# Kernel tuning notes

Measured on AMD Instinct MI355X. Metric: run time of the kernel, lower is better.

The kernel has to match this reference:

```python
import jax, jax.numpy as jnp
import numpy as np

TOPK = 13
ALPHA = 1.0
BETA = 6.0
NUM_CLASSES = 80
EPS = 1e-9


def _make_boxes(key, shape, max_half):
    # shape = (..., 4): build valid x1y1x2y2 boxes inside a 640x640 image
    kc, ks = jax.random.split(key)
    centers = jax.random.uniform(kc, shape[:-1] + (2,), minval=30.0, maxval=610.0)
    halves = jax.random.uniform(ks, shape[:-1] + (2,), minval=2.0, maxval=max_half)
    return jnp.concatenate([centers - halves, centers + halves], axis=-1)


def setup_inputs() -> dict:
    key = jax.random.key(0)
    k1, k2, k3, k4, k5 = jax.random.split(key, 5)
    B, L, C, n = 16, 8400, NUM_CLASSES, 128
    pred_scores = jax.random.uniform(k1, (B, L, C), dtype=jnp.float32)
    pred_bboxes = _make_boxes(k2, (B, L, 4), 60.0)
    anchor_points = jax.random.uniform(k3, (L, 2), minval=0.0, maxval=640.0)
    gt_labels = jax.random.randint(k4, (B, n), 0, C, dtype=jnp.int32)
    gt_bboxes = _make_boxes(k5, (B, n, 4), 120.0)
    pad_gt_mask = jnp.ones((B, n, 1), dtype=jnp.float32)
    return {"pred_scores": pred_scores, "pred_bboxes": pred_bboxes,
            "anchor_points": anchor_points, "gt_labels": gt_labels,
            "gt_bboxes": gt_bboxes, "pad_gt_mask": pad_gt_mask}


def _batch_iou(box1, box2, eps=1e-9):
    # box1: [B, n, 4], box2: [B, L, 4] -> iou [B, n, L]
    b1 = box1[:, :, None]  # [B,n,1,4]
    b2 = box2[:, None]     # [B,1,L,4]
    x1y1 = jnp.maximum(b1[..., 0:2], b2[..., 0:2])
    x2y2 = jnp.minimum(b1[..., 2:4], b2[..., 2:4])
    overlap = jnp.prod(jnp.clip(x2y2 - x1y1, 0.0), axis=-1)
    area1 = jnp.prod(jnp.clip(b1[..., 2:4] - b1[..., 0:2], 0.0), axis=-1)
    area2 = jnp.prod(jnp.clip(b2[..., 2:4] - b2[..., 0:2], 0.0), axis=-1)
    return overlap / (area1 + area2 - overlap + eps)


def _points_in_bboxes(points, bboxes, eps=EPS):
    # points: [L,2], bboxes: [B,n,4] -> [B,n,L] float
    x = points[None, None, :, 0]
    y = points[None, None, :, 1]
    xmin = bboxes[..., 0:1]; ymin = bboxes[..., 1:2]
    xmax = bboxes[..., 2:3]; ymax = bboxes[..., 3:4]
    l = x - xmin; t = y - ymin; r = xmax - x; b = ymax - y
    d = jnp.minimum(jnp.minimum(l, t), jnp.minimum(r, b))
    return (d > eps).astype(bboxes.dtype)


def _gather_topk(metrics, topk, topk_mask):
    # metrics: [B,n,L] -> one-hot membership of per-gt topk anchors [B,n,L]
    L = metrics.shape[-1]
    _, topk_idxs = jax.lax.top_k(metrics, topk)          # [B,n,topk]
    is_in_topk = jax.nn.one_hot(topk_idxs, L, dtype=metrics.dtype).sum(-2)
    return is_in_topk * topk_mask


def reference(pred_scores, pred_bboxes, anchor_points, gt_labels, gt_bboxes, pad_gt_mask):
    B, n, _ = gt_bboxes.shape
    L = pred_bboxes.shape[1]
    # pairwise IoU between gts and predicted boxes: [B,n,L]
    ious = _batch_iou(gt_bboxes, pred_bboxes)
    # per-gt class scores gathered from pred_scores: [B,n,L]
    scores_cl = jnp.transpose(pred_scores, (0, 2, 1))                 # [B,C,L]
    bbox_cls_scores = jnp.take_along_axis(scores_cl, gt_labels[:, :, None].astype(jnp.int32), axis=1)
    # task-aligned metric
    alignment = (bbox_cls_scores ** ALPHA) * (ious ** BETA)
    is_in_gts = _points_in_bboxes(anchor_points, gt_bboxes)           # [B,n,L]
    is_in_topk = _gather_topk(alignment * is_in_gts, TOPK, pad_gt_mask)
    mask_positive = is_in_topk * is_in_gts * pad_gt_mask              # [B,n,L]
    # resolve anchors assigned to multiple gts: keep max-IoU gt
    mask_pos_sum = mask_positive.sum(-2)                              # [B,L]
    is_max_iou = jnp.transpose(jax.nn.one_hot(jnp.argmax(ious, axis=-2), n, dtype=ious.dtype), (0, 2, 1))
    mask_positive = jnp.where((mask_pos_sum[:, None, :] > 1), is_max_iou, mask_positive)
    mask_pos_sum = mask_positive.sum(-2)
    # assignment
    assigned_gt_index = jnp.argmax(mask_positive, axis=-2)            # [B,L]
    flat_idx = assigned_gt_index + jnp.arange(B, dtype=assigned_gt_index.dtype)[:, None] * n
    assigned_labels = jnp.reshape(gt_labels, (-1,))[flat_idx]
    assigned_labels = jnp.where(mask_pos_sum > 0, assigned_labels, NUM_CLASSES)
    assigned_bboxes = jnp.reshape(gt_bboxes, (-1, 4))[flat_idx]       # [B,L,4]
    assigned_scores = jax.nn.one_hot(assigned_labels, NUM_CLASSES + 1, dtype=pred_scores.dtype)[..., :NUM_CLASSES]
    # rescale scores by normalized alignment metric
    align_m = alignment * mask_positive
    max_metric = align_m.max(-1, keepdims=True)                       # [B,n,1]
    max_iou = (ious * mask_positive).max(-1, keepdims=True)           # [B,n,1]
    align_m = (align_m / (max_metric + EPS)) * max_iou
    assigned_scores = assigned_scores * align_m.max(-2)[..., None]    # [B,L,C]
    return assigned_labels, assigned_bboxes, assigned_scores
```

## Files before the change

kernel.cpp:

```cpp
#include <hip/hip_runtime.h>
#include <stdint.h>

#define BB   16
#define NGT  128
#define LL   8400
#define CC   80
#define KTOP 13
#define CAP  1024
#define FEPS 1e-9f

typedef float vfloat4 __attribute__((ext_vector_type(4)));

__device__ __forceinline__ float iou_f(float4 g, float4 p) {
    float ix0 = fmaxf(g.x, p.x);
    float iy0 = fmaxf(g.y, p.y);
    float ix1 = fminf(g.z, p.z);
    float iy1 = fminf(g.w, p.w);
    float ow = fmaxf(ix1 - ix0, 0.0f);
    float oh = fmaxf(iy1 - iy0, 0.0f);
    float ov = ow * oh;
    float a1 = fmaxf(g.z - g.x, 0.0f) * fmaxf(g.w - g.y, 0.0f);
    float a2 = fmaxf(p.z - p.x, 0.0f) * fmaxf(p.w - p.y, 0.0f);
    return ov / (a1 + a2 - ov + FEPS);
}

#define SORT2(a,b) { unsigned long long _t=(a), _u=(b); (a)=(_u>_t)?_u:_t; (b)=(_u>_t)?_t:_u; }
#define INSERT13(key) do { unsigned long long _k=(key); if (_k > k12) { k12=_k; \
    SORT2(k11,k12) SORT2(k10,k11) SORT2(k9,k10) SORT2(k8,k9) SORT2(k7,k8) \
    SORT2(k6,k7)  SORT2(k5,k6)  SORT2(k4,k5) SORT2(k3,k4) SORT2(k2,k3) \
    SORT2(k1,k2)  SORT2(k0,k1) } } while(0)
#define POP13() { k0=k1;k1=k2;k2=k3;k3=k4;k4=k5;k5=k6;k6=k7;k7=k8;k8=k9;k9=k10;k10=k11;k11=k12;k12=0ull; }

__global__ __launch_bounds__(256) void cand_kernel(
    const float*  __restrict__ pred_scores,
    const float4* __restrict__ pred_bboxes,
    const float2* __restrict__ anchors,
    const int*    __restrict__ gt_labels,
    const float4* __restrict__ gt_bboxes,
    unsigned long long* __restrict__ records,
    int* __restrict__ cand_cnt)
{
    int b  = blockIdx.y;
    int zi = blockIdx.z;
    int j  = blockIdx.x * 256 + threadIdx.x;

    __shared__ float4 gbox[8];
    __shared__ int    glab[8];
    if (threadIdx.x < 8) {
        gbox[threadIdx.x] = gt_bboxes[b * NGT + zi * 8 + threadIdx.x];
        glab[threadIdx.x] = gt_labels[b * NGT + zi * 8 + threadIdx.x];
    }
    __syncthreads();
    if (j >= LL) return;

    float2 ap = anchors[j];
    float4 p  = pred_bboxes[(size_t)b * LL + j];
    const float* srow = pred_scores + ((size_t)b * LL + j) * CC;

    unsigned mask = 0;
#pragma unroll
    for (int u = 0; u < 8; ++u) {
        float4 gg = gbox[u];
        float d  = fminf(fminf(ap.x - gg.x, ap.y - gg.y),
                         fminf(gg.z - ap.x, gg.w - ap.y));
        float io = iou_f(gg, p);
        mask |= ((d > FEPS) && (io > 0.0f)) ? (1u << u) : 0u;
    }

    while (mask) {
        int u = __ffs(mask) - 1;
        mask &= mask - 1;
        float4 gg = gbox[u];
        float io  = iou_f(gg, p);
        float s   = srow[glab[u]];
        float i2  = io * io;
        float met = s * (i2 * i2 * i2);
        if (met > 0.0f) {
            int rrow = b * NGT + zi * 8 + u;
            int slot = atomicAdd(cand_cnt + rrow, 1);
            if (slot < CAP)
                records[(size_t)rrow * CAP + slot] =
                    ((unsigned long long)__float_as_uint(met) << 32)
                    | (unsigned)(~(unsigned)j);
        }
    }
}

__global__ __launch_bounds__(64) void select_kernel(
    const float*  __restrict__ pred_scores,
    const float4* __restrict__ pred_bboxes,
    const float2* __restrict__ anchors,
    const int*    __restrict__ gt_labels,
    const float4* __restrict__ gt_bboxes,
    const unsigned long long* __restrict__ records,
    const int* __restrict__ cand_cnt,
    int force_fallback,
    int* __restrict__ claim_count,
    int* __restrict__ claimant)
{
    int lane = threadIdx.x;
    int row  = blockIdx.x;
    int b    = row >> 7;
    int i_gt = row & (NGT - 1);

    float4 g = gt_bboxes[row];
    unsigned long long k0=0,k1=0,k2=0,k3=0,k4=0,k5=0,k6=0,k7=0,k8=0,k9=0,k10=0,k11=0,k12=0;

    int cnt = cand_cnt[row];
    if (force_fallback || cnt > CAP) {
        int label = gt_labels[row];
        const float*  sc = pred_scores + (size_t)b * LL * CC + label;
        const float4* pb = pred_bboxes + (size_t)b * LL;
        for (int j = lane; j < LL; j += 64) {
            float2 ap = anchors[j];
            float d = fminf(fminf(ap.x - g.x, ap.y - g.y),
                            fminf(g.z - ap.x, g.w - ap.y));
            if (d > FEPS) {
                float4 p = pb[j];
                float iou = iou_f(g, p);
                if (iou > 0.0f) {
                    float s  = sc[(size_t)j * CC];
                    float i2 = iou * iou;
                    float met = s * (i2 * i2 * i2);
                    if (met > 0.0f)
                        INSERT13(((unsigned long long)__float_as_uint(met) << 32)
                                 | (unsigned)(~(unsigned)j));
                }
            }
        }
    } else {
        const unsigned long long* rr = records + (size_t)row * CAP;
        for (int t = lane; t < cnt; t += 64)
            INSERT13(rr[t]);
    }

    unsigned long long winner = 0ull;
    for (int r = 0; r < KTOP; ++r) {
        unsigned long long head = k0;
        unsigned long long m = head;
#pragma unroll
        for (int off = 1; off < 64; off <<= 1) {
            unsigned long long o = __shfl_xor(m, off, 64);
            if (o > m) m = o;
        }
        if (head == m && m != 0ull) {
            POP13();
        }
        if (lane == r) winner = m;
    }

    int jwv = -1;
    if (lane < KTOP && winner != 0ull)
        jwv = (int)(~(unsigned)(winner & 0xFFFFFFFFull));

    bool marked = false;
    for (int r = 0; r < KTOP; ++r) {
        int jv = __shfl(jwv, r, 64);
        if (jv == lane) marked = true;
    }
    unsigned long long nonpos = ~__ballot(marked);
    int P = __popcll(__ballot(jwv >= 0));

    int base = b * LL;
    if (jwv >= 0) {
        atomicAdd(claim_count + base + jwv, 1);
        atomicMax(claimant + base + jwv, i_gt);
    }
    if (lane >= P && lane < KTOP) {
        unsigned long long mask = nonpos;
        for (int t = 0; t < lane - P; ++t) mask &= mask - 1ull;
        int jf = __ffsll(mask) - 1;
        float2 ap = anchors[jf];
        float d = fminf(fminf(ap.x - g.x, ap.y - g.y),
                        fminf(g.z - ap.x, g.w - ap.y));
        if (d > FEPS) {
            atomicAdd(claim_count + base + jf, 1);
            atomicMax(claimant + base + jf, i_gt);
        }
    }
}

__global__ __launch_bounds__(256) void resolve_kernel(
    const float*  __restrict__ pred_scores,
    const float4* __restrict__ pred_bboxes,
    const int*    __restrict__ gt_labels,
    const float4* __restrict__ gt_bboxes,
    const int*    __restrict__ claim_count,
    const int*    __restrict__ claimant,
    int*      __restrict__ assigned_gt,
    float*    __restrict__ align_anchor,
    unsigned* __restrict__ max_metric,
    unsigned* __restrict__ max_iou,
    float*    __restrict__ out_labels,
    float4*   __restrict__ out_bboxes)
{
    int b = blockIdx.y;
    int j = blockIdx.x * 256 + threadIdx.x;

    __shared__ float4 gbox[NGT];
    __shared__ int    glab[NGT];
    if (threadIdx.x < NGT) {
        gbox[threadIdx.x] = gt_bboxes[b * NGT + threadIdx.x];
        glab[threadIdx.x] = gt_labels[b * NGT + threadIdx.x];
    }
    __syncthreads();
    if (j >= LL) return;

    int idx = b * LL + j;
    int cnt = claim_count[idx];
    int g = -1;
    float4 p = pred_bboxes[(size_t)b * LL + j];

    if (cnt == 1) {
        g = claimant[idx];
    } else if (cnt > 1) {
        float best = -1.0f;
        int   bi   = 0;
        for (int i = 0; i < NGT; ++i) {
            float iou = iou_f(gbox[i], p);
            if (iou > best) { best = iou; bi = i; }
        }
        g = bi;
    }
    assigned_gt[idx] = g;

    int label; float4 bb;
    if (g >= 0) {
        float iou = iou_f(gbox[g], p);
        float s   = pred_scores[((size_t)b * LL + j) * CC + glab[g]];
        float i2  = iou * iou;
        float al  = s * (i2 * i2 * i2);
        align_anchor[idx] = al;
        atomicMax(max_metric + b * NGT + g, __float_as_uint(al));
        atomicMax(max_iou    + b * NGT + g, __float_as_uint(iou));
        label = glab[g];
        bb    = gbox[g];
    } else {
        label = CC;
        bb    = gbox[0];
    }
    out_labels[idx] = (float)label;
    out_bboxes[idx] = bb;
}

__global__ __launch_bounds__(256) void score_kernel(
    const int*    __restrict__ gt_labels,
    const int*    __restrict__ assigned_gt,
    const float*  __restrict__ align_anchor,
    const unsigned* __restrict__ max_metric,
    const unsigned* __restrict__ max_iou,
    float*  __restrict__ out_scores)
{
    __shared__ int   s_lab[64];
    __shared__ float s_f[64];

    if (threadIdx.x < 64) {
        int t = blockIdx.x * 64 + threadIdx.x;
        int b = t / LL;
        int g = assigned_gt[t];
        int label = CC;
        float f = 0.0f;
        if (g >= 0) {
            label = gt_labels[b * NGT + g];
            float mm = __uint_as_float(max_metric[b * NGT + g]);
            float mi = __uint_as_float(max_iou[b * NGT + g]);
            f = align_anchor[t] / (mm + FEPS) * mi;
        }
        s_lab[threadIdx.x] = label;
        s_f[threadIdx.x]   = f;
    }
    __syncthreads();

    vfloat4* outs = (vfloat4*)(out_scores + (size_t)blockIdx.x * 64 * CC);
#pragma unroll
    for (int k = 0; k < 5; ++k) {
        int i = k * 256 + threadIdx.x;
        int anchor = i / (CC / 4);
        int c4     = i % (CC / 4);
        int lab    = s_lab[anchor];
        vfloat4 v = {0.f, 0.f, 0.f, 0.f};
        int rel = lab - c4 * 4;
        if (rel >= 0 && rel < 4) v[rel] = s_f[anchor];
        __builtin_nontemporal_store(v, outs + i);
    }
}

extern "C" void kernel_launch(void* const* d_in, const int* in_sizes, int n_in,
                              void* d_out, int out_size, void* d_ws, size_t ws_size,
                              hipStream_t stream)
{
    const float*  pred_scores = (const float*)d_in[0];
    const float4* pred_bboxes = (const float4*)d_in[1];
    const float2* anchors     = (const float2*)d_in[2];
    const int*    gt_labels   = (const int*)d_in[3];
    const float4* gt_bboxes   = (const float4*)d_in[4];

    char* w = (char*)d_ws;
    int*      claim_count  = (int*)(w);
    int*      claimant     = (int*)(w + 537600);
    unsigned* max_metric   = (unsigned*)(w + 1075200);
    unsigned* max_iou      = (unsigned*)(w + 1083392);
    int*      cand_cnt     = (int*)(w + 1091584);
    int*      assigned_gt  = (int*)(w + 1099776);
    float*    align_anchor = (float*)(w + 1637376);
    unsigned long long* records = (unsigned long long*)(w + 2174976);

    const size_t WS_NEEDED = 2174976ull + (size_t)BB * NGT * CAP * 8ull;
    int force_fallback = (ws_size < WS_NEEDED) ? 1 : 0;

    float*  out        = (float*)d_out;
    float*  out_labels = out;
    float4* out_bboxes = (float4*)(out + (size_t)BB * LL);
    float*  out_scores = out + (size_t)BB * LL * 5;

    (void)hipMemsetAsync(w, 0, 1099776, stream);

    if (!force_fallback) {
        dim3 gridG((LL + 255) / 256, BB, 16);
        cand_kernel<<<gridG, 256, 0, stream>>>(
            pred_scores, pred_bboxes, anchors, gt_labels, gt_bboxes,
            records, cand_cnt);
    }

    select_kernel<<<BB * NGT, 64, 0, stream>>>(
        pred_scores, pred_bboxes, anchors, gt_labels, gt_bboxes,
        records, cand_cnt, force_fallback, claim_count, claimant);

    dim3 gridC((LL + 255) / 256, BB);
    resolve_kernel<<<gridC, 256, 0, stream>>>(
        pred_scores, pred_bboxes, gt_labels, gt_bboxes,
        claim_count, claimant, assigned_gt, align_anchor, max_metric, max_iou,
        out_labels, out_bboxes);

    score_kernel<<<(BB * LL) / 64, 256, 0, stream>>>(
        gt_labels, assigned_gt, align_anchor, max_metric, max_iou, out_scores);
}
```

Baseline: 92.33 us.

## Remap candidate kernel to one thread per anchor-GT pair; use plain score stores

The candidate kernel's thread mapping changes from one thread per anchor looping over 8 GTs in shared memory to one thread per (anchor, GT) pair across all 128 GTs. The shared-memory staging and barrier go away, and the serial per-anchor loop is spread across lanes, at the cost of redundant anchor and pred_box loads and divergent branches inside each wavefront. Score output also switches from nontemporal stores to ordinary vector stores, which changes how the large output write interacts with the cache.

```diff
diff --git a/kernel.cpp b/kernel.cpp
--- a/kernel.cpp
+++ b/kernel.cpp
@@ -40,48 +40,31 @@
     unsigned long long* __restrict__ records,
     int* __restrict__ cand_cnt)
 {
-    int b  = blockIdx.y;
-    int zi = blockIdx.z;
-    int j  = blockIdx.x * 256 + threadIdx.x;
-
-    __shared__ float4 gbox[8];
-    __shared__ int    glab[8];
-    if (threadIdx.x < 8) {
-        gbox[threadIdx.x] = gt_bboxes[b * NGT + zi * 8 + threadIdx.x];
-        glab[threadIdx.x] = gt_labels[b * NGT + zi * 8 + threadIdx.x];
-    }
-    __syncthreads();
-    if (j >= LL) return;
-
-    float2 ap = anchors[j];
-    float4 p  = pred_bboxes[(size_t)b * LL + j];
-    const float* srow = pred_scores + ((size_t)b * LL + j) * CC;
-
-    unsigned mask = 0;
-#pragma unroll
-    for (int u = 0; u < 8; ++u) {
-        float4 gg = gbox[u];
-        float d  = fminf(fminf(ap.x - gg.x, ap.y - gg.y),
-                         fminf(gg.z - ap.x, gg.w - ap.y));
-        float io = iou_f(gg, p);
-        mask |= ((d > FEPS) && (io > 0.0f)) ? (1u << u) : 0u;
-    }
-
-    while (mask) {
-        int u = __ffs(mask) - 1;
-        mask &= mask - 1;
-        float4 gg = gbox[u];
-        float io  = iou_f(gg, p);
-        float s   = srow[glab[u]];
-        float i2  = io * io;
-        float met = s * (i2 * i2 * i2);
-        if (met > 0.0f) {
-            int rrow = b * NGT + zi * 8 + u;
-            int slot = atomicAdd(cand_cnt + rrow, 1);
-            if (slot < CAP)
-                records[(size_t)rrow * CAP + slot] =
-                    ((unsigned long long)__float_as_uint(met) << 32)
-                    | (unsigned)(~(unsigned)j);
+    int b = blockIdx.y;
+    int p = blockIdx.x * 256 + threadIdx.x;
+    int j = p >> 7;
+    int i = p & (NGT - 1);
+
+    float2 ap  = anchors[j];
+    float4 pbx = pred_bboxes[(size_t)b * LL + j];
+    float4 gg  = gt_bboxes[b * NGT + i];
+
+    float d = fminf(fminf(ap.x - gg.x, ap.y - gg.y),
+                    fminf(gg.z - ap.x, gg.w - ap.y));
+    if (d > FEPS) {
+        float io = iou_f(gg, pbx);
+        if (io > 0.0f) {
+            float s  = pred_scores[((size_t)b * LL + j) * CC + gt_labels[b * NGT + i]];
+            float i2 = io * io;
+            float met = s * (i2 * i2 * i2);
+            if (met > 0.0f) {
+                int rrow = b * NGT + i;
+                int slot = atomicAdd(cand_cnt + rrow, 1);
+                if (slot < CAP)
+                    records[(size_t)rrow * CAP + slot] =
+                        ((unsigned long long)__float_as_uint(met) << 32)
+                        | (unsigned)(~(unsigned)j);
+            }
         }
     }
 }
@@ -281,7 +264,7 @@
         vfloat4 v = {0.f, 0.f, 0.f, 0.f};
         int rel = lab - c4 * 4;
         if (rel >= 0 && rel < 4) v[rel] = s_f[anchor];
-        __builtin_nontemporal_store(v, outs + i);
+        outs[i] = v;
     }
 }
 
@@ -316,7 +299,7 @@
     (void)hipMemsetAsync(w, 0, 1099776, stream);
 
     if (!force_fallback) {
-        dim3 gridG((LL + 255) / 256, BB, 16);
+        dim3 gridG(LL * NGT / 256, BB);
         cand_kernel<<<gridG, 256, 0, stream>>>(
             pred_scores, pred_bboxes, anchors, gt_labels, gt_bboxes,
             records, cand_cnt);
```

New measurement: 125.3 us. +35.7%, slower.
